# Kernel tuning notes

Hardware: AMD Instinct MI355X
Metric: run time of the kernel (lower is better)

Reference implementation:

```python
import jax, jax.numpy as jnp
import numpy as np


def setup_inputs() -> dict:
    key = jax.random.key(0)
    k1, k2 = jax.random.split(key)
    H, D, N = 1, 256, 65536        # (heads=1, embedding_dim, num_tokens)
    C = 1024                       # num_embeddings (codebook size)
    inputs = jax.random.normal(k1, (H, D, N), dtype=jnp.float32)
    embedding = jax.random.normal(k2, (H, C, D), dtype=jnp.float32)
    return {"inputs": inputs, "embedding": embedding}


COMMITMENT_COST = 0.25


def reference(inputs, embedding):
    # inputs: (h, d, n) -> flat: (h, n, d)
    flat = jnp.transpose(inputs, (0, 2, 1))
    # negative euclidean distance (matches -torch.cdist, p=2)
    x2 = jnp.sum(flat * flat, axis=-1, keepdims=True)            # (h, n, 1)
    e2 = jnp.sum(embedding * embedding, axis=-1)[:, None, :]     # (h, 1, c)
    xe = jnp.einsum('hnd,hcd->hnc', flat, embedding)             # (h, n, c)
    d2 = jnp.maximum(x2 + e2 - 2.0 * xe, 0.0)
    distances = -jnp.sqrt(d2)                                    # (h, n, c)
    encoding_indices = jnp.argmax(distances, axis=2)             # (h, n)
    # gather codebook vectors: h == 1
    quantized = jnp.take(embedding[0], encoding_indices[0], axis=0)[None]  # (h, n, d)
    commit_loss = jnp.mean((jax.lax.stop_gradient(quantized) - flat) ** 2)
    loss = COMMITMENT_COST * commit_loss
    # straight-through estimator
    quantized_st = flat + jax.lax.stop_gradient(quantized - flat)
    out = jnp.transpose(quantized_st, (0, 2, 1))                 # (h, d, n)
    return out, encoding_indices, loss, distances
```

## Files before the change

### kernel.cpp

```cpp
#include <hip/hip_runtime.h>
#include <math.h>

#define N_TOK 65536
#define D_DIM 256
#define C_NUM 1024

#define OUT_OFF   0
#define IDX_OFF   (D_DIM * N_TOK)
#define LOSS_OFF  (IDX_OFF + N_TOK)
#define DIST_OFF  (LOSS_OFF + 1)

#define EH_OFF_F  0
#define EL_OFF_F  131072
#define E2_OFF_F  262144
#define PART_OFF_F 263168
#define NPART 4096

typedef __attribute__((ext_vector_type(8))) short bf16x8;
typedef __attribute__((ext_vector_type(4))) float f32x4;

static __device__ __forceinline__ unsigned short f2bf(float f) {
  unsigned int u = __float_as_uint(f);
  unsigned int r = (u + 0x7fffu + ((u >> 16) & 1u)) >> 16;
  return (unsigned short)r;
}
static __device__ __forceinline__ float bf2f(unsigned short h) {
  return __uint_as_float(((unsigned int)h) << 16);
}

__global__ __launch_bounds__(256) void kA_prep(const float* __restrict__ X,
                                               const float* __restrict__ E,
                                               float* __restrict__ out) {
  const int bid = blockIdx.x, tid = threadIdx.x;
  if (bid < 256) {
    const int n = bid * 256 + tid;
    float s = 0.0f;
#pragma unroll 8
    for (int d = 0; d < D_DIM; ++d) {
      float v = X[(size_t)d * N_TOK + n];
      s = fmaf(v, v, s);
    }
    out[IDX_OFF + n] = s;
  } else {
    unsigned short* EhG = (unsigned short*)(out + EH_OFF_F);
    unsigned short* ElG = (unsigned short*)(out + EL_OFF_F);
    const int lane = tid & 63, w = tid >> 6;
#pragma unroll 1
    for (int cc = 0; cc < 16; ++cc) {
      const int c = (bid - 256) * 64 + w * 16 + cc;
      const float4 v = *(const float4*)(E + (size_t)c * D_DIM + lane * 4);
      unsigned short h0 = f2bf(v.x), h1 = f2bf(v.y), h2 = f2bf(v.z), h3 = f2bf(v.w);
      unsigned short l0 = f2bf(v.x - bf2f(h0)), l1 = f2bf(v.y - bf2f(h1));
      unsigned short l2 = f2bf(v.z - bf2f(h2)), l3 = f2bf(v.w - bf2f(h3));
      ushort4 hv = make_ushort4(h0, h1, h2, h3);
      ushort4 lv = make_ushort4(l0, l1, l2, l3);
      *(ushort4*)(EhG + (size_t)c * D_DIM + lane * 4) = hv;
      *(ushort4*)(ElG + (size_t)c * D_DIM + lane * 4) = lv;
      float s = v.x * v.x + v.y * v.y + v.z * v.z + v.w * v.w;
#pragma unroll
      for (int off = 32; off; off >>= 1) s += __shfl_down(s, off, 64);
      if (lane == 0) out[E2_OFF_F + c] = s;
    }
  }
}

#define TM 64
#define TC 256
#define BK 32
#define XS 40

__global__ __launch_bounds__(256) void k2_dist(const float* __restrict__ X,
                                               float* __restrict__ out) {
  __shared__ unsigned short xh[TM * XS];
  __shared__ unsigned short xl[TM * XS];

  const unsigned short* __restrict__ EhG = (const unsigned short*)(out + EH_OFF_F);
  const unsigned short* __restrict__ ElG = (const unsigned short*)(out + EL_OFF_F);

  const int tid = threadIdx.x;
  const int lane = tid & 63, wave = tid >> 6;
  const int c0 = blockIdx.x * TC;
  const int n0 = blockIdx.y * TM;
  const int wc = c0 + wave * 64;
  const int m = lane & 15;
  const int q = lane >> 4;

  f32x4 acc[4][4];
#pragma unroll
  for (int i = 0; i < 4; ++i)
#pragma unroll
    for (int t = 0; t < 4; ++t) acc[i][t] = (f32x4){0.f, 0.f, 0.f, 0.f};

  const int sn = lane;
  const int kg = wave;

#pragma unroll 1
  for (int kb = 0; kb < D_DIM; kb += BK) {
    const float* xp = X + (size_t)(kb + kg * 8) * N_TOK + n0 + sn;
    float xv[8];
#pragma unroll
    for (int j = 0; j < 8; ++j) xv[j] = xp[(size_t)j * N_TOK];
    unsigned short hh[8], ll[8];
#pragma unroll
    for (int j = 0; j < 8; ++j) {
      hh[j] = f2bf(xv[j]);
      ll[j] = f2bf(xv[j] - bf2f(hh[j]));
    }
    *(bf16x8*)&xh[sn * XS + kg * 8] = *(bf16x8*)hh;
    *(bf16x8*)&xl[sn * XS + kg * 8] = *(bf16x8*)ll;
    __syncthreads();

    bf16x8 bh[4], bl[4];
#pragma unroll
    for (int t = 0; t < 4; ++t) {
      const size_t eoff = (size_t)(wc + t * 16 + m) * D_DIM + kb + q * 8;
      bh[t] = *(const bf16x8*)(EhG + eoff);
      bl[t] = *(const bf16x8*)(ElG + eoff);
    }
    bf16x8 ah[4], al[4];
#pragma unroll
    for (int i = 0; i < 4; ++i) {
      const int ro = (i * 16 + m) * XS + q * 8;
      ah[i] = *(const bf16x8*)&xh[ro];
      al[i] = *(const bf16x8*)&xl[ro];
    }
#pragma unroll
    for (int i = 0; i < 4; ++i)
#pragma unroll
      for (int t = 0; t < 4; ++t) {
        acc[i][t] = __builtin_amdgcn_mfma_f32_16x16x32_bf16(ah[i], bh[t], acc[i][t], 0, 0, 0);
        acc[i][t] = __builtin_amdgcn_mfma_f32_16x16x32_bf16(ah[i], bl[t], acc[i][t], 0, 0, 0);
        acc[i][t] = __builtin_amdgcn_mfma_f32_16x16x32_bf16(al[i], bh[t], acc[i][t], 0, 0, 0);
      }
    __syncthreads();
  }

  float e2v[4];
#pragma unroll
  for (int t = 0; t < 4; ++t) e2v[t] = out[E2_OFF_F + wc + t * 16 + m];

#pragma unroll
  for (int i = 0; i < 4; ++i) {
#pragma unroll
    for (int r = 0; r < 4; ++r) {
      const int tok = n0 + i * 16 + q * 4 + r;
      const float x2v = out[IDX_OFF + tok];
      const size_t row = DIST_OFF + (size_t)tok * C_NUM;
#pragma unroll
      for (int t = 0; t < 4; ++t) {
        float d2 = fmaf(-2.0f, acc[i][t][r], x2v + e2v[t]);
        d2 = fmaxf(d2, 0.0f);
        out[row + wc + t * 16 + m] = -sqrtf(d2);
      }
    }
  }
}

#define MARGIN 0.01f

__global__ __launch_bounds__(256) void k3_argmax(const float* __restrict__ X,
                                                 const float* __restrict__ E,
                                                 float* __restrict__ out) {
  __shared__ float lsum[4];
  const int tid = threadIdx.x, lane = tid & 63, w = tid >> 6;
  float wloss = 0.0f;

#pragma unroll 1
  for (int it = 0; it < 4; ++it) {
    const int n = blockIdx.x * 16 + w * 4 + it;
    const float* row = out + DIST_OFF + (size_t)n * C_NUM;

    float v[16];
    float best = -3.4e38f;
    int bi = 0x7fffffff;
#pragma unroll
    for (int j = 0; j < 16; ++j) {
      v[j] = row[j * 64 + lane];
      if (v[j] > best) { best = v[j]; bi = j * 64 + lane; }
    }
#pragma unroll
    for (int off = 32; off; off >>= 1) {
      const float ov = __shfl_xor(best, off, 64);
      const int oi = __shfl_xor(bi, off, 64);
      if (ov > best || (ov == best && oi < bi)) { best = ov; bi = oi; }
    }
    const float thr = best - MARGIN;
    unsigned long long masks[16];
    int total = 0;
#pragma unroll
    for (int j = 0; j < 16; ++j) {
      masks[j] = __ballot(v[j] > thr);
      total += __popcll(masks[j]);
    }
    float best_d2 = best * best;
    int best_idx = bi;
    if (total > 1) {
      best_d2 = 3.4e38f;
      best_idx = 0x7fffffff;
      for (int j = 0; j < 16; ++j) {
        unsigned long long mm = masks[j];
        while (mm) {
          const int l = __ffsll((long long)mm) - 1;
          mm &= mm - 1;
          const int c = j * 64 + l;
          float sx = 0.f, se = 0.f, sxe = 0.f;
#pragma unroll
          for (int r = 0; r < 4; ++r) {
            const int d = r * 64 + lane;
            const float xv = X[(size_t)d * N_TOK + n];
            const float ev = E[(size_t)c * D_DIM + d];
            sx = fmaf(xv, xv, sx);
            se = fmaf(ev, ev, se);
            sxe = fmaf(xv, ev, sxe);
          }
          float d2 = fmaf(-2.f, sxe, sx + se);
#pragma unroll
          for (int off = 32; off; off >>= 1) d2 += __shfl_xor(d2, off, 64);
          d2 = fmaxf(d2, 0.f);
          if (d2 < best_d2 || (d2 == best_d2 && c < best_idx)) {
            best_d2 = d2; best_idx = c;
          }
        }
      }
    }
    if (lane == 0) out[IDX_OFF + n] = (float)best_idx;
    wloss += best_d2;
  }
  if (lane == 0) lsum[w] = wloss;
  __syncthreads();
  if (tid == 0)
    out[PART_OFF_F + blockIdx.x] = lsum[0] + lsum[1] + lsum[2] + lsum[3];
}

__global__ __launch_bounds__(256) void k3b_loss(float* __restrict__ out) {
  __shared__ float red[4];
  const int tid = threadIdx.x, lane = tid & 63, w = tid >> 6;
  float s = 0.0f;
#pragma unroll
  for (int i = 0; i < NPART / 256; ++i) s += out[PART_OFF_F + i * 256 + tid];
#pragma unroll
  for (int off = 32; off; off >>= 1) s += __shfl_down(s, off, 64);
  if (lane == 0) red[w] = s;
  __syncthreads();
  if (tid == 0)
    out[LOSS_OFF] = (red[0] + red[1] + red[2] + red[3]) *
                    (0.25f / ((float)N_TOK * (float)D_DIM));
}

__global__ __launch_bounds__(256) void k4_gather(const float* __restrict__ E,
                                                 float* __restrict__ out) {
  const int g = blockIdx.x * 256 + threadIdx.x;
  const int n = g * 4;
  const int i0 = (int)out[IDX_OFF + n + 0];
  const int i1 = (int)out[IDX_OFF + n + 1];
  const int i2 = (int)out[IDX_OFF + n + 2];
  const int i3 = (int)out[IDX_OFF + n + 3];
  const float* e0 = E + (size_t)i0 * D_DIM;
  const float* e1 = E + (size_t)i1 * D_DIM;
  const float* e2 = E + (size_t)i2 * D_DIM;
  const float* e3 = E + (size_t)i3 * D_DIM;
  const int d0 = blockIdx.y * 32;
#pragma unroll 4
  for (int d = d0; d < d0 + 32; ++d) {
    float4 wv = make_float4(e0[d], e1[d], e2[d], e3[d]);
    *(float4*)&out[(size_t)d * N_TOK + n] = wv;
  }
}

extern "C" void kernel_launch(void* const* d_in, const int* in_sizes, int n_in,
                              void* d_out, int out_size, void* d_ws, size_t ws_size,
                              hipStream_t stream) {
  const float* X = (const float*)d_in[0];
  const float* E = (const float*)d_in[1];
  float* out = (float*)d_out;

  hipLaunchKernelGGL(kA_prep, dim3(272), dim3(256), 0, stream, X, E, out);
  hipLaunchKernelGGL(k2_dist, dim3(C_NUM / TC, N_TOK / TM), dim3(256), 0, stream,
                     X, out);
  hipLaunchKernelGGL(k3_argmax, dim3(N_TOK / 16), dim3(256), 0, stream, X, E, out);
  hipLaunchKernelGGL(k3b_loss, dim3(1), dim3(256), 0, stream, out);
  hipLaunchKernelGGL(k4_gather, dim3(N_TOK / 4 / 256, 8), dim3(256), 0, stream,
                     E, out);
}
```

Measured before the change: 673.8 us.

## Double-buffer X tiles with register prefetch and remap blocks per XCD

```diff
diff --git a/kernel.cpp b/kernel.cpp
--- a/kernel.cpp
+++ b/kernel.cpp
@@ -71,16 +71,23 @@
 
 __global__ __launch_bounds__(256) void k2_dist(const float* __restrict__ X,
                                                float* __restrict__ out) {
-  __shared__ unsigned short xh[TM * XS];
-  __shared__ unsigned short xl[TM * XS];
+  __shared__ __align__(16) unsigned short xh[2][TM * XS];
+  __shared__ __align__(16) unsigned short xl[2][TM * XS];
 
   const unsigned short* __restrict__ EhG = (const unsigned short*)(out + EH_OFF_F);
   const unsigned short* __restrict__ ElG = (const unsigned short*)(out + EL_OFF_F);
 
   const int tid = threadIdx.x;
   const int lane = tid & 63, wave = tid >> 6;
-  const int c0 = blockIdx.x * TC;
-  const int n0 = blockIdx.y * TM;
+
+  const int bid = blockIdx.x;
+  const int xcd = bid & 7;
+  const int slot = bid >> 3;
+  const int bx = slot & 3;
+  const int by = xcd * 128 + (slot >> 2);
+  const int c0 = bx * TC;
+  const int n0 = by * TM;
+
   const int wc = c0 + wave * 64;
   const int m = lane & 15;
   const int q = lane >> 4;
@@ -94,21 +101,16 @@
   const int sn = lane;
   const int kg = wave;
 
+  float xv[8];
+  {
+    const float* xp = X + (size_t)(kg * 8) * N_TOK + n0 + sn;
+#pragma unroll
+    for (int j = 0; j < 8; ++j) xv[j] = xp[(size_t)j * N_TOK];
+  }
+
 #pragma unroll 1
   for (int kb = 0; kb < D_DIM; kb += BK) {
-    const float* xp = X + (size_t)(kb + kg * 8) * N_TOK + n0 + sn;
-    float xv[8];
-#pragma unroll
-    for (int j = 0; j < 8; ++j) xv[j] = xp[(size_t)j * N_TOK];
-    unsigned short hh[8], ll[8];
-#pragma unroll
-    for (int j = 0; j < 8; ++j) {
-      hh[j] = f2bf(xv[j]);
-      ll[j] = f2bf(xv[j] - bf2f(hh[j]));
-    }
-    *(bf16x8*)&xh[sn * XS + kg * 8] = *(bf16x8*)hh;
-    *(bf16x8*)&xl[sn * XS + kg * 8] = *(bf16x8*)ll;
-    __syncthreads();
+    const int p = (kb >> 5) & 1;
 
     bf16x8 bh[4], bl[4];
 #pragma unroll
@@ -117,12 +119,30 @@
       bh[t] = *(const bf16x8*)(EhG + eoff);
       bl[t] = *(const bf16x8*)(ElG + eoff);
     }
+
+    unsigned short hh[8], ll[8];
+#pragma unroll
+    for (int j = 0; j < 8; ++j) {
+      hh[j] = f2bf(xv[j]);
+      ll[j] = f2bf(xv[j] - bf2f(hh[j]));
+    }
+    *(bf16x8*)&xh[p][sn * XS + kg * 8] = *(bf16x8*)hh;
+    *(bf16x8*)&xl[p][sn * XS + kg * 8] = *(bf16x8*)ll;
+
+    if (kb + BK < D_DIM) {
+      const float* xp = X + (size_t)(kb + BK + kg * 8) * N_TOK + n0 + sn;
+#pragma unroll
+      for (int j = 0; j < 8; ++j) xv[j] = xp[(size_t)j * N_TOK];
+    }
+
+    __syncthreads();
+
     bf16x8 ah[4], al[4];
 #pragma unroll
     for (int i = 0; i < 4; ++i) {
       const int ro = (i * 16 + m) * XS + q * 8;
-      ah[i] = *(const bf16x8*)&xh[ro];
-      al[i] = *(const bf16x8*)&xl[ro];
+      ah[i] = *(const bf16x8*)&xh[p][ro];
+      al[i] = *(const bf16x8*)&xl[p][ro];
     }
 #pragma unroll
     for (int i = 0; i < 4; ++i)
@@ -132,7 +152,6 @@
         acc[i][t] = __builtin_amdgcn_mfma_f32_16x16x32_bf16(ah[i], bl[t], acc[i][t], 0, 0, 0);
         acc[i][t] = __builtin_amdgcn_mfma_f32_16x16x32_bf16(al[i], bh[t], acc[i][t], 0, 0, 0);
       }
-    __syncthreads();
   }
 
   float e2v[4];
@@ -275,8 +294,8 @@
   float* out = (float*)d_out;
 
   hipLaunchKernelGGL(kA_prep, dim3(272), dim3(256), 0, stream, X, E, out);
-  hipLaunchKernelGGL(k2_dist, dim3(C_NUM / TC, N_TOK / TM), dim3(256), 0, stream,
-                     X, out);
+  hipLaunchKernelGGL(k2_dist, dim3((C_NUM / TC) * (N_TOK / TM)), dim3(256), 0,
+                     stream, X, out);
   hipLaunchKernelGGL(k3_argmax, dim3(N_TOK / 16), dim3(256), 0, stream, X, E, out);
   hipLaunchKernelGGL(k3b_loss, dim3(1), dim3(256), 0, stream, out);
   hipLaunchKernelGGL(k4_gather, dim3(N_TOK / 4 / 256, 8), dim3(256), 0, stream,
```

Result: faster. 618.8 us (-8.2%).
